# Optimization experiments

Hardware: AMD Instinct MI355X
Metric: run time of the kernel (lower is better)

The kernel has to match this reference:

```python
import jax, jax.numpy as jnp
import numpy as np

E = 500_000
NODE_DIM = 128
EDGE_DIM = 128
GLOB_DIM = 64
NUM_GRAPHS = 64
HIDDEN = 4 * EDGE_DIM  # 512
IN_DIM = 2 * NODE_DIM + EDGE_DIM + GLOB_DIM  # 448
EPS = 1e-5


def setup_inputs() -> dict:
    key = jax.random.key(0)
    ks = jax.random.split(key, 12)
    src = jax.random.normal(ks[0], (E, NODE_DIM), dtype=jnp.float32)
    dest = jax.random.normal(ks[1], (E, NODE_DIM), dtype=jnp.float32)
    edge_attr = jax.random.normal(ks[2], (E, EDGE_DIM), dtype=jnp.float32)
    u = jax.random.normal(ks[3], (NUM_GRAPHS, GLOB_DIM), dtype=jnp.float32)
    batch = jnp.sort(jax.random.randint(ks[4], (E,), 0, NUM_GRAPHS, dtype=jnp.int32))
    # MLP params (kaiming-ish scale)
    W1 = jax.random.normal(ks[5], (IN_DIM, HIDDEN), dtype=jnp.float32) / np.sqrt(IN_DIM)
    b1 = jnp.zeros((HIDDEN,), dtype=jnp.float32)
    W2 = jax.random.normal(ks[6], (HIDDEN, EDGE_DIM), dtype=jnp.float32) / np.sqrt(HIDDEN)
    b2 = jnp.zeros((EDGE_DIM,), dtype=jnp.float32)
    # GraphNorm params
    gn_weight = jnp.ones((EDGE_DIM,), dtype=jnp.float32)
    gn_bias = jnp.zeros((EDGE_DIM,), dtype=jnp.float32)
    mean_scale = jnp.ones((EDGE_DIM,), dtype=jnp.float32)
    return {"src": src, "dest": dest, "edge_attr": edge_attr, "u": u, "batch": batch,
            "W1": W1, "b1": b1, "W2": W2, "b2": b2,
            "gn_weight": gn_weight, "gn_bias": gn_bias, "mean_scale": mean_scale}


def _graph_norm(x, batch, weight, bias, mean_scale):
    # per-graph mean
    cnt = jax.ops.segment_sum(jnp.ones((x.shape[0],), x.dtype), batch, num_segments=NUM_GRAPHS)
    cnt = jnp.maximum(cnt, 1.0)[:, None]  # [G,1]
    mean = jax.ops.segment_sum(x, batch, num_segments=NUM_GRAPHS) / cnt  # [G,D]
    out = x - mean[batch] * mean_scale
    var = jax.ops.segment_sum(out * out, batch, num_segments=NUM_GRAPHS) / cnt  # [G,D]
    std = jnp.sqrt(var + EPS)
    return out / std[batch] * weight + bias


def reference(src, dest, edge_attr, u, batch, W1, b1, W2, b2, gn_weight, gn_bias, mean_scale):
    # gather per-graph globals + concat: [E, 2*node+edge+glob]
    h = jnp.concatenate([src, dest, edge_attr, u[batch]], axis=1)
    h = jax.nn.relu(h @ W1 + b1) @ W2 + b2  # [E, edge_dim]
    out = _graph_norm(h + edge_attr, batch, gn_weight, gn_bias, mean_scale)
    return out  # dropout is identity in eval / p=0.0
```

## Files before the change

### kernel.cpp

```cpp
#include <hip/hip_runtime.h>
#include <hip/hip_bf16.h>
#include <stdint.h>

#define E_EDGES   500000
#define MBLK      32
#define NBLK      15625
#define EPSV      1e-5f
#define YOFF      32768

typedef unsigned short u16;
typedef __attribute__((ext_vector_type(8))) short short8;
typedef __attribute__((ext_vector_type(4))) float f32x4;
typedef __attribute__((ext_vector_type(2))) uint32_t u32x2;

__device__ __forceinline__ u16 f2bf(float f) {
  __hip_bfloat16 h = __float2bfloat16(f);
  return *(u16*)&h;
}
__device__ __forceinline__ uint32_t pk2bf(float lo, float hi) {
  return (uint32_t)f2bf(lo) | ((uint32_t)f2bf(hi) << 16);
}

__global__ void prep_weights(const float* __restrict__ W1, const float* __restrict__ W2,
                             u16* __restrict__ w1f, u16* __restrict__ w2f) {
  int idx = blockIdx.x * blockDim.x + threadIdx.x;
  if (idx < 32*14*64) {
    int lane = idx & 63; int t = idx >> 6; int k32 = t % 14; int n16 = t / 14;
    int n = n16*16 + (lane & 15); int k0 = k32*32 + (lane >> 4)*8;
    short8 pk;
#pragma unroll
    for (int j = 0; j < 8; ++j) pk[j] = (short)f2bf(W1[(size_t)(k0 + j)*512 + n]);
    *(short8*)&w1f[(size_t)idx * 8] = pk;
  } else if (idx < 32*14*64 + 8*16*64) {
    int i2 = idx - 32*14*64;
    int lane = i2 & 63; int t = i2 >> 6; int k32 = t % 16; int n16 = t / 16;
    int n = n16*16 + (lane & 15); int k0 = k32*32 + (lane >> 4)*8;
    short8 pk;
#pragma unroll
    for (int j = 0; j < 8; ++j) pk[j] = (short)f2bf(W2[(size_t)(k0 + j)*128 + n]);
    *(short8*)&w2f[(size_t)i2 * 8] = pk;
  }
}

#define SWZ16(row, byte) ((byte) ^ (((row) & 7) << 4))

__global__ __launch_bounds__(256, 4)
void fused_kernel(const float* __restrict__ srcp, const float* __restrict__ destp,
                  const float* __restrict__ edgep, const float* __restrict__ up,
                  const int* __restrict__ batch, const float* __restrict__ b1,
                  const float* __restrict__ b2,
                  const u16* __restrict__ w1f, const u16* __restrict__ w2f,
                  float* __restrict__ outp,
                  float* __restrict__ sums0, float* __restrict__ sums2,
                  float* __restrict__ cntsh, int nshard) {
  const int tid  = threadIdx.x;
  const int lane = tid & 63;
  const int w    = tid >> 6;
  const int l15  = lane & 15, l4 = lane >> 4;

  __shared__ __align__(16) char ldsb[49152];

  const long grow0 = (long)blockIdx.x * MBLK;

  {
    const int srow = tid >> 3;
    const int c8   = (tid & 7) * 8;
    const long sgrow = grow0 + srow;
    const int  bat = batch[sgrow];
#pragma unroll
    for (int j = 0; j < 7; ++j) {
      const float* sp;
      if (j == 0)      sp = srcp  + sgrow*128 + c8;
      else if (j == 1) sp = srcp  + sgrow*128 + 64 + c8;
      else if (j == 2) sp = destp + sgrow*128 + c8;
      else if (j == 3) sp = destp + sgrow*128 + 64 + c8;
      else if (j == 4) sp = edgep + sgrow*128 + c8;
      else if (j == 5) sp = edgep + sgrow*128 + 64 + c8;
      else             sp = up + (size_t)bat*64 + c8;
      f32x4 t0 = *(const f32x4*)(sp);
      f32x4 t1 = *(const f32x4*)(sp + 4);
      u32x2 lohi0 = (u32x2){pk2bf(t0[0], t0[1]), pk2bf(t0[2], t0[3])};
      u32x2 lohi1 = (u32x2){pk2bf(t1[0], t1[1]), pk2bf(t1[2], t1[3])};
      char* dst = ldsb + srow*896 + SWZ16(srow, (j*64 + c8)*2);
      *(u32x2*)(dst)     = lohi0;
      *(u32x2*)(dst + 8) = lohi1;
    }
  }
  __syncthreads();

  f32x4 acc1[2][8];
#pragma unroll
  for (int nj = 0; nj < 8; ++nj) {
    float bv = b1[(w*8 + nj)*16 + l15];
    acc1[0][nj] = (f32x4){bv, bv, bv, bv};
    acc1[1][nj] = (f32x4){bv, bv, bv, bv};
  }

#pragma unroll 2
  for (int k32 = 0; k32 < 14; ++k32) {
    short8 a[2], b[8];
#pragma unroll
    for (int mi = 0; mi < 2; ++mi) {
      int row = mi*16 + l15;
      a[mi] = *(const short8*)(ldsb + row*896 + SWZ16(row, k32*64 + l4*16));
    }
#pragma unroll
    for (int nj = 0; nj < 8; ++nj)
      b[nj] = *(const short8*)&w1f[((size_t)((w*8 + nj)*14 + k32)*64 + lane)*8];
#pragma unroll
    for (int mi = 0; mi < 2; ++mi)
#pragma unroll
      for (int nj = 0; nj < 8; ++nj)
        acc1[mi][nj] = __builtin_amdgcn_mfma_f32_16x16x32_bf16(a[mi], b[nj], acc1[mi][nj], 0, 0, 0);
  }
  __syncthreads();

#pragma unroll
  for (int nj = 0; nj < 8; ++nj) {
    int n = (w*8 + nj)*16 + l15;
#pragma unroll
    for (int mi = 0; mi < 2; ++mi)
#pragma unroll
      for (int rr = 0; rr < 4; ++rr) {
        int row = mi*16 + l4*4 + rr;
        *(u16*)(ldsb + row*1024 + SWZ16(row, n*2)) = f2bf(fmaxf(acc1[mi][nj][rr], 0.f));
      }
  }
  __syncthreads();

  const int c4    = tid & 31;
  const int rbase = tid >> 5;
  f32x4 ebuf[4];
#pragma unroll
  for (int p = 0; p < 4; ++p)
    ebuf[p] = *(const f32x4*)(edgep + (grow0 + rbase + p*8)*128 + c4*4);

  f32x4 acc2[2][2];
#pragma unroll
  for (int nj = 0; nj < 2; ++nj) {
    float bv = b2[(w*2 + nj)*16 + l15];
    acc2[0][nj] = (f32x4){bv, bv, bv, bv};
    acc2[1][nj] = (f32x4){bv, bv, bv, bv};
  }

#pragma unroll 4
  for (int kb = 0; kb < 16; ++kb) {
    short8 hb[2], wfr[2];
#pragma unroll
    for (int mi = 0; mi < 2; ++mi) {
      int row = mi*16 + l15;
      hb[mi] = *(const short8*)(ldsb + row*1024 + SWZ16(row, kb*64 + l4*16));
    }
#pragma unroll
    for (int nj = 0; nj < 2; ++nj)
      wfr[nj] = *(const short8*)&w2f[(((size_t)((w*2 + nj)*16 + kb))*64 + lane)*8];
#pragma unroll
    for (int mi = 0; mi < 2; ++mi)
#pragma unroll
      for (int nj = 0; nj < 2; ++nj)
        acc2[mi][nj] = __builtin_amdgcn_mfma_f32_16x16x32_bf16(hb[mi], wfr[nj], acc2[mi][nj], 0, 0, 0);
  }

#pragma unroll
  for (int mi = 0; mi < 2; ++mi)
#pragma unroll
    for (int nj = 0; nj < 2; ++nj) {
      int col = (w*2 + nj)*16 + l15;
#pragma unroll
      for (int rr = 0; rr < 4; ++rr) {
        int row = mi*16 + l4*4 + rr;
        *(float*)(ldsb + YOFF + row*512 + SWZ16(row, col*4)) = acc2[mi][nj][rr];
      }
    }

  const int g0 = batch[grow0];
  const int g1 = batch[grow0 + MBLK - 1];
  const int sh = blockIdx.x & (nshard - 1);

  if (g0 == g1) {
    float s[2] = {0.f, 0.f}, s2[2] = {0.f, 0.f};
#pragma unroll
    for (int nj = 0; nj < 2; ++nj) {
      int col = (w*2 + nj)*16 + l15;
#pragma unroll
      for (int mi = 0; mi < 2; ++mi)
#pragma unroll
        for (int rr = 0; rr < 4; ++rr) {
          int row = mi*16 + l4*4 + rr;
          float y = acc2[mi][nj][rr] + edgep[(grow0 + row)*128 + col];
          s[nj] += y; s2[nj] += y*y;
        }
    }
#pragma unroll
    for (int m = 16; m <= 32; m <<= 1) {
#pragma unroll
      for (int nj = 0; nj < 2; ++nj) {
        s[nj]  += __shfl_xor(s[nj],  m);
        s2[nj] += __shfl_xor(s2[nj], m);
      }
    }
    if (lane < 16) {
#pragma unroll
      for (int nj = 0; nj < 2; ++nj) {
        int col = (w*2 + nj)*16 + l15;
        atomicAdd(&sums0[(size_t)sh*8192 + g0*128 + col], s[nj]);
        atomicAdd(&sums2[(size_t)sh*8192 + g0*128 + col], s2[nj]);
      }
    }
    if (tid == 0) atomicAdd(&cntsh[sh*64 + g0], (float)MBLK);
  }
  __syncthreads();

  if (g0 == g1) {
#pragma unroll
    for (int p = 0; p < 4; ++p) {
      int row = rbase + p*8;
      f32x4 y = *(const f32x4*)(ldsb + YOFF + row*512 + SWZ16(row, c4*16));
      y = y + ebuf[p];
      *(f32x4*)(outp + (grow0 + row)*128 + c4*4) = y;
    }
  } else {
    f32x4 s = (f32x4){0,0,0,0}, s2v = (f32x4){0,0,0,0};
    float rc = 0.f; int gcur = -1;
#pragma unroll
    for (int p = 0; p < 4; ++p) {
      int row = rbase + p*8;
      int g = batch[grow0 + row];
      if (g != gcur) {
        if (gcur >= 0) {
#pragma unroll
          for (int c = 0; c < 4; ++c) {
            atomicAdd(&sums0[(size_t)sh*8192 + gcur*128 + c4*4 + c], s[c]);
            atomicAdd(&sums2[(size_t)sh*8192 + gcur*128 + c4*4 + c], s2v[c]);
          }
          if (c4 == 0) atomicAdd(&cntsh[sh*64 + gcur], rc);
        }
        gcur = g; s = (f32x4){0,0,0,0}; s2v = (f32x4){0,0,0,0}; rc = 0.f;
      }
      f32x4 y = *(const f32x4*)(ldsb + YOFF + row*512 + SWZ16(row, c4*16));
      y = y + ebuf[p];
      *(f32x4*)(outp + (grow0 + row)*128 + c4*4) = y;
      s = s + y; s2v = s2v + y*y; rc += 1.f;
    }
#pragma unroll
    for (int c = 0; c < 4; ++c) {
      atomicAdd(&sums0[(size_t)sh*8192 + gcur*128 + c4*4 + c], s[c]);
      atomicAdd(&sums2[(size_t)sh*8192 + gcur*128 + c4*4 + c], s2v[c]);
    }
    if (c4 == 0) atomicAdd(&cntsh[sh*64 + gcur], rc);
  }
}

__global__ void finalize_kernel(const float* __restrict__ sums0, const float* __restrict__ sums2,
                                const float* __restrict__ cntsh, int nshard,
                                const float* __restrict__ gnw, const float* __restrict__ gnb,
                                const float* __restrict__ ms,
                                float* __restrict__ scale, float* __restrict__ shift) {
  int idx = blockIdx.x*blockDim.x + threadIdx.x;
  if (idx >= 64*128) return;
  int g = idx >> 7, d = idx & 127;
  float s = 0.f, s2 = 0.f, c = 0.f;
  for (int sh = 0; sh < nshard; ++sh) {
    s  += sums0[(size_t)sh*8192 + idx];
    s2 += sums2[(size_t)sh*8192 + idx];
    c  += cntsh[sh*64 + g];
  }
  c = fmaxf(c, 1.0f);
  float mean = s / c;
  float mm = mean * ms[d];
  float var = fmaxf(s2 / c - 2.f*mm*mean + mm*mm, 0.f);
  float sc = gnw[d] / sqrtf(var + EPSV);
  scale[idx] = sc;
  shift[idx] = gnb[d] - mm*sc;
}

__global__ void norm_kernel(float* __restrict__ y, const int* __restrict__ batch,
                            const float* __restrict__ scale, const float* __restrict__ shift) {
  long i = (long)blockIdx.x*blockDim.x + threadIdx.x;
  const long n4 = (long)E_EDGES * 32;
  long stride = (long)gridDim.x*blockDim.x;
  for (; i < n4; i += stride) {
    long row = i >> 5;
    int dq = (int)(i & 31) << 2;
    int g = batch[row];
    f32x4 v = *(f32x4*)(y + i*4);
    f32x4 sc = *(const f32x4*)(scale + g*128 + dq);
    f32x4 sh = *(const f32x4*)(shift + g*128 + dq);
    v = v*sc + sh;
    *(f32x4*)(y + i*4) = v;
  }
}

extern "C" void kernel_launch(void* const* d_in, const int* in_sizes, int n_in,
                              void* d_out, int out_size, void* d_ws, size_t ws_size,
                              hipStream_t stream) {
  const float* srcp  = (const float*)d_in[0];
  const float* destp = (const float*)d_in[1];
  const float* edgep = (const float*)d_in[2];
  const float* up    = (const float*)d_in[3];
  const int*   batch = (const int*)d_in[4];
  const float* W1    = (const float*)d_in[5];
  const float* b1    = (const float*)d_in[6];
  const float* W2    = (const float*)d_in[7];
  const float* b2    = (const float*)d_in[8];
  const float* gnw   = (const float*)d_in[9];
  const float* gnb   = (const float*)d_in[10];
  const float* ms    = (const float*)d_in[11];
  float* outp = (float*)d_out;

  char* ws = (char*)d_ws;
  u16*   w1f   = (u16*)(ws + 0);
  u16*   w2f   = (u16*)(ws + 458752);
  float* scale = (float*)(ws + 589824);
  float* shift = (float*)(ws + 622592);
  float* cntsh = (float*)(ws + 655360);
  int nshard = 32;
  while (nshard > 1 && 663552 + (size_t)nshard*65536 > ws_size) nshard >>= 1;
  float* sums0 = (float*)(ws + 663552);
  float* sums2 = (float*)(ws + 663552 + (size_t)nshard*32768);

  hipMemsetAsync(ws + 655360, 0, 8192 + (size_t)nshard*65536, stream);
  prep_weights<<<dim3(144), dim3(256), 0, stream>>>(W1, W2, w1f, w2f);

  fused_kernel<<<dim3(NBLK), dim3(256), 0, stream>>>(srcp, destp, edgep, up, batch,
                                                     b1, b2, w1f, w2f, outp,
                                                     sums0, sums2, cntsh, nshard);

  finalize_kernel<<<dim3(32), dim3(256), 0, stream>>>(sums0, sums2, cntsh, nshard,
                                                      gnw, gnb, ms, scale, shift);
  norm_kernel<<<dim3(2048), dim3(256), 0, stream>>>(outp, batch, scale, shift);
}
```

Measured before the change: 629.4 us.

## Swap second GEMM operands to write output directly from registers

The second MFMA now takes the weight fragment as the A operand, so the accumulator lanes hold four consecutive columns of one row. Each lane adds edge_attr and writes the output as a 16-byte vector straight from registers, so the LDS staging of Y, the extra barrier and the 16KB of Y buffer are gone (LDS drops to 32KB, which may allow more resident blocks). Statistics are reduced with shuffles over 16 lanes. Blocks that span a graph boundary now do one atomic per element, which is costlier, but such blocks are rare.

```diff
diff --git a/kernel.cpp b/kernel.cpp
--- a/kernel.cpp
+++ b/kernel.cpp
@@ -6,7 +6,6 @@
 #define MBLK      32
 #define NBLK      15625
 #define EPSV      1e-5f
-#define YOFF      32768
 
 typedef unsigned short u16;
 typedef __attribute__((ext_vector_type(8))) short short8;
@@ -58,7 +57,8 @@
   const int w    = tid >> 6;
   const int l15  = lane & 15, l4 = lane >> 4;
 
-  __shared__ __align__(16) char ldsb[49152];
+  __shared__ __align__(16) u16 lds[32*512];
+  char* ldsb = (char*)lds;
 
   const long grow0 = (long)blockIdx.x * MBLK;
 
@@ -128,19 +128,20 @@
   }
   __syncthreads();
 
-  const int c4    = tid & 31;
-  const int rbase = tid >> 5;
-  f32x4 ebuf[4];
-#pragma unroll
-  for (int p = 0; p < 4; ++p)
-    ebuf[p] = *(const f32x4*)(edgep + (grow0 + rbase + p*8)*128 + c4*4);
+  f32x4 ebuf[2][2];
+#pragma unroll
+  for (int mi = 0; mi < 2; ++mi)
+#pragma unroll
+    for (int nj2 = 0; nj2 < 2; ++nj2)
+      ebuf[mi][nj2] = *(const f32x4*)(edgep + (grow0 + mi*16 + l15)*128
+                                            + (w*2 + nj2)*16 + l4*4);
 
   f32x4 acc2[2][2];
 #pragma unroll
-  for (int nj = 0; nj < 2; ++nj) {
-    float bv = b2[(w*2 + nj)*16 + l15];
-    acc2[0][nj] = (f32x4){bv, bv, bv, bv};
-    acc2[1][nj] = (f32x4){bv, bv, bv, bv};
+  for (int nj2 = 0; nj2 < 2; ++nj2) {
+    f32x4 bv = *(const f32x4*)&b2[(w*2 + nj2)*16 + l4*4];
+    acc2[0][nj2] = bv;
+    acc2[1][nj2] = bv;
   }
 
 #pragma unroll 4
@@ -152,102 +153,71 @@
       hb[mi] = *(const short8*)(ldsb + row*1024 + SWZ16(row, kb*64 + l4*16));
     }
 #pragma unroll
-    for (int nj = 0; nj < 2; ++nj)
-      wfr[nj] = *(const short8*)&w2f[(((size_t)((w*2 + nj)*16 + kb))*64 + lane)*8];
+    for (int nj2 = 0; nj2 < 2; ++nj2)
+      wfr[nj2] = *(const short8*)&w2f[(((size_t)((w*2 + nj2)*16 + kb))*64 + lane)*8];
 #pragma unroll
     for (int mi = 0; mi < 2; ++mi)
 #pragma unroll
-      for (int nj = 0; nj < 2; ++nj)
-        acc2[mi][nj] = __builtin_amdgcn_mfma_f32_16x16x32_bf16(hb[mi], wfr[nj], acc2[mi][nj], 0, 0, 0);
-  }
-
-#pragma unroll
-  for (int mi = 0; mi < 2; ++mi)
-#pragma unroll
-    for (int nj = 0; nj < 2; ++nj) {
-      int col = (w*2 + nj)*16 + l15;
-#pragma unroll
-      for (int rr = 0; rr < 4; ++rr) {
-        int row = mi*16 + l4*4 + rr;
-        *(float*)(ldsb + YOFF + row*512 + SWZ16(row, col*4)) = acc2[mi][nj][rr];
-      }
-    }
+      for (int nj2 = 0; nj2 < 2; ++nj2)
+        acc2[mi][nj2] = __builtin_amdgcn_mfma_f32_16x16x32_bf16(wfr[nj2], hb[mi], acc2[mi][nj2], 0, 0, 0);
+  }
 
   const int g0 = batch[grow0];
   const int g1 = batch[grow0 + MBLK - 1];
   const int sh = blockIdx.x & (nshard - 1);
 
   if (g0 == g1) {
-    float s[2] = {0.f, 0.f}, s2[2] = {0.f, 0.f};
-#pragma unroll
-    for (int nj = 0; nj < 2; ++nj) {
-      int col = (w*2 + nj)*16 + l15;
-#pragma unroll
-      for (int mi = 0; mi < 2; ++mi)
-#pragma unroll
-        for (int rr = 0; rr < 4; ++rr) {
-          int row = mi*16 + l4*4 + rr;
-          float y = acc2[mi][nj][rr] + edgep[(grow0 + row)*128 + col];
-          s[nj] += y; s2[nj] += y*y;
+    f32x4 s[2], s2[2];
+#pragma unroll
+    for (int nj2 = 0; nj2 < 2; ++nj2) { s[nj2] = (f32x4){0,0,0,0}; s2[nj2] = (f32x4){0,0,0,0}; }
+#pragma unroll
+    for (int mi = 0; mi < 2; ++mi)
+#pragma unroll
+      for (int nj2 = 0; nj2 < 2; ++nj2) {
+        f32x4 y = acc2[mi][nj2] + ebuf[mi][nj2];
+        *(f32x4*)(outp + (grow0 + mi*16 + l15)*128 + (w*2 + nj2)*16 + l4*4) = y;
+        s[nj2] = s[nj2] + y; s2[nj2] = s2[nj2] + y*y;
+      }
+#pragma unroll
+    for (int m = 1; m <= 8; m <<= 1) {
+#pragma unroll
+      for (int nj2 = 0; nj2 < 2; ++nj2) {
+#pragma unroll
+        for (int c = 0; c < 4; ++c) {
+          s[nj2][c]  += __shfl_xor(s[nj2][c],  m);
+          s2[nj2][c] += __shfl_xor(s2[nj2][c], m);
         }
-    }
-#pragma unroll
-    for (int m = 16; m <= 32; m <<= 1) {
-#pragma unroll
-      for (int nj = 0; nj < 2; ++nj) {
-        s[nj]  += __shfl_xor(s[nj],  m);
-        s2[nj] += __shfl_xor(s2[nj], m);
-      }
-    }
-    if (lane < 16) {
-#pragma unroll
-      for (int nj = 0; nj < 2; ++nj) {
-        int col = (w*2 + nj)*16 + l15;
-        atomicAdd(&sums0[(size_t)sh*8192 + g0*128 + col], s[nj]);
-        atomicAdd(&sums2[(size_t)sh*8192 + g0*128 + col], s2[nj]);
+      }
+    }
+    if (l15 == 0) {
+#pragma unroll
+      for (int nj2 = 0; nj2 < 2; ++nj2) {
+        int col = (w*2 + nj2)*16 + l4*4;
+#pragma unroll
+        for (int c = 0; c < 4; ++c) {
+          atomicAdd(&sums0[(size_t)sh*8192 + g0*128 + col + c], s[nj2][c]);
+          atomicAdd(&sums2[(size_t)sh*8192 + g0*128 + col + c], s2[nj2][c]);
+        }
       }
     }
     if (tid == 0) atomicAdd(&cntsh[sh*64 + g0], (float)MBLK);
-  }
-  __syncthreads();
-
-  if (g0 == g1) {
-#pragma unroll
-    for (int p = 0; p < 4; ++p) {
-      int row = rbase + p*8;
-      f32x4 y = *(const f32x4*)(ldsb + YOFF + row*512 + SWZ16(row, c4*16));
-      y = y + ebuf[p];
-      *(f32x4*)(outp + (grow0 + row)*128 + c4*4) = y;
-    }
   } else {
-    f32x4 s = (f32x4){0,0,0,0}, s2v = (f32x4){0,0,0,0};
-    float rc = 0.f; int gcur = -1;
-#pragma unroll
-    for (int p = 0; p < 4; ++p) {
-      int row = rbase + p*8;
-      int g = batch[grow0 + row];
-      if (g != gcur) {
-        if (gcur >= 0) {
-#pragma unroll
-          for (int c = 0; c < 4; ++c) {
-            atomicAdd(&sums0[(size_t)sh*8192 + gcur*128 + c4*4 + c], s[c]);
-            atomicAdd(&sums2[(size_t)sh*8192 + gcur*128 + c4*4 + c], s2v[c]);
-          }
-          if (c4 == 0) atomicAdd(&cntsh[sh*64 + gcur], rc);
+#pragma unroll
+    for (int mi = 0; mi < 2; ++mi) {
+      int g = batch[grow0 + mi*16 + l15];
+#pragma unroll
+      for (int nj2 = 0; nj2 < 2; ++nj2) {
+        f32x4 y = acc2[mi][nj2] + ebuf[mi][nj2];
+        *(f32x4*)(outp + (grow0 + mi*16 + l15)*128 + (w*2 + nj2)*16 + l4*4) = y;
+        int col = (w*2 + nj2)*16 + l4*4;
+#pragma unroll
+        for (int c = 0; c < 4; ++c) {
+          atomicAdd(&sums0[(size_t)sh*8192 + g*128 + col + c], y[c]);
+          atomicAdd(&sums2[(size_t)sh*8192 + g*128 + col + c], y[c]*y[c]);
         }
-        gcur = g; s = (f32x4){0,0,0,0}; s2v = (f32x4){0,0,0,0}; rc = 0.f;
-      }
-      f32x4 y = *(const f32x4*)(ldsb + YOFF + row*512 + SWZ16(row, c4*16));
-      y = y + ebuf[p];
-      *(f32x4*)(outp + (grow0 + row)*128 + c4*4) = y;
-      s = s + y; s2v = s2v + y*y; rc += 1.f;
-    }
-#pragma unroll
-    for (int c = 0; c < 4; ++c) {
-      atomicAdd(&sums0[(size_t)sh*8192 + gcur*128 + c4*4 + c], s[c]);
-      atomicAdd(&sums2[(size_t)sh*8192 + gcur*128 + c4*4 + c], s2v[c]);
-    }
-    if (c4 == 0) atomicAdd(&cntsh[sh*64 + gcur], rc);
+      }
+      if (w == 0 && l4 == 0) atomicAdd(&cntsh[sh*64 + g], 1.0f);
+    }
   }
 }
 
```

New measurement: 657.0 us. 4.4% more time.
